# Performance work log

Hardware: AMD Instinct MI355X
Metric: run time of the kernel (lower is better)

## Reference

```python
import jax, jax.numpy as jnp
import numpy as np

B, NPG = 64, 512          # graphs, nodes per graph
N_TOTAL = B * NPG
LIG = 128                 # ligand nodes per graph (segment 0); rest are protein (segment 1)
BOX = 40.0                # Angstrom box for random coords -> realistic radius-graph density
INTER_CUTOFF = 10.0       # normalize_coord is identity (scale=1)
INTRA_CUTOFF = 8.0


def setup_inputs() -> dict:
    key = jax.random.key(0)
    X = jax.random.uniform(key, (N_TOTAL, 1, 3), dtype=jnp.float32) * BOX
    batch_id = jnp.repeat(jnp.arange(B, dtype=jnp.int32), NPG)
    local = jnp.tile(jnp.arange(NPG, dtype=jnp.int32), B)
    segment_id = (local >= LIG).astype(jnp.int32)
    is_global = jnp.logical_or(local == 0, local == LIG)  # one global node per segment
    return {"X": X, "batch_id": batch_id, "segment_id": segment_id, "is_global": is_global}


def _radial_edges(X, src_dst, cutoff):
    # src_dst: [E, 2] node indices; X: [N, C, 3], channel 0 holds coords
    p = X[:, 0][src_dst]                              # [E, 2, 3]
    dist = jnp.linalg.norm(p[:, 0] - p[:, 1], axis=-1)
    return src_dst[dist <= cutoff].T                  # [2, E']


def reference(X, batch_id, segment_id, is_global):
    N = batch_id.shape[0]
    nB = int(batch_id[-1]) + 1
    lengths = jax.ops.segment_sum(jnp.ones_like(batch_id), batch_id, num_segments=nB)
    max_n = int(jnp.max(lengths))
    offsets = jnp.concatenate([jnp.zeros((1,), lengths.dtype), jnp.cumsum(lengths)[:-1]])
    gni = jnp.arange(N)
    gni2lni = gni - offsets[batch_id]                 # local node index within its graph

    # Dense [N, max_n] same-batch mask via cumsum trick (O(N*max_n))
    same_bid = jnp.zeros((N, max_n), jnp.float32)
    same_bid = same_bid.at[gni, lengths[batch_id] - 1].set(1.0)
    same_bid = 1.0 - jnp.cumsum(same_bid, axis=-1)
    same_bid = jnp.concatenate([jnp.ones((N, 1), jnp.float32), same_bid[:, :-1]], axis=-1)
    same_bid = same_bid.at[gni, gni2lni].set(0.0)     # remove self edges

    row, col = jnp.nonzero(same_bid)                  # all same-graph candidate pairs
    col = col + offsets[batch_id[row]]                # local col -> global node index

    row_global = is_global[row]
    col_global = is_global[col]
    not_global = jnp.logical_not(jnp.logical_or(row_global, col_global))
    row_seg = segment_id[row]
    col_seg = segment_id[col]

    # intra-protein context edges (segment 1, within 8A)
    sel = (row_seg == col_seg) & (row_seg == 1) & not_global
    ctx_edges = _radial_edges(X, jnp.stack([row[sel], col[sel]], axis=1), INTRA_CUTOFF)

    # inter ligand-protein edges (within 10A)
    sel = (row_seg != col_seg) & not_global
    ir, ic = row[sel], col[sel]
    inter_edges = _radial_edges(X, jnp.stack([ir, ic], axis=1), INTER_CUTOFF)
    if inter_edges.shape[1] == 0:
        inter_edges = jnp.array([[ir[0], ic[0]], [ic[0], ir[0]]], dtype=inter_edges.dtype)

    reduced_inter_edge_batchid = batch_id[inter_edges[0][inter_edges[0] < inter_edges[1]]]
    reduced_inter_edge_offsets = offsets[reduced_inter_edge_batchid]

    # global<->same-segment edges and global<->global edges appended to context
    sel = (row_seg == col_seg) & jnp.logical_not(not_global)
    global_normal = jnp.stack([row[sel], col[sel]])
    sel = row_global & col_global
    global_global = jnp.stack([row[sel], col[sel]])
    ctx_edges = jnp.concatenate([ctx_edges, global_normal, global_global], axis=1)

    return ctx_edges, inter_edges, reduced_inter_edge_batchid, reduced_inter_edge_offsets
```

## Files before the change

kernel.cpp:

```cpp
#include <hip/hip_runtime.h>

#define NB 64
#define NPG 512
#define LIG 128
#define NBLK 2048
#define RPB 16
#define THREADS 256
typedef unsigned long long ull;

__device__ __forceinline__ float dist2(float dx, float dy, float dz) {
    return __fadd_rn(__fadd_rn(__fmul_rn(dx, dx), __fmul_rn(dy, dy)), __fmul_rn(dz, dz));
}
#define T10 __uint_as_float(0x42C80001u)
#define T8  __uint_as_float(0x42800001u)

__global__ __launch_bounds__(THREADS) void count_kernel(const float* __restrict__ X,
                                                        ull* __restrict__ gmask,
                                                        int* __restrict__ bp) {
    __shared__ float s[NPG * 3];
    __shared__ ull smask[RPB * 8];
    __shared__ int rcs[RPB], ris[RPB];
    const int b = blockIdx.x;
    const int g = b >> 5;
    const int sg = b & 31;
    const int t = threadIdx.x;
    const int lane = t & 63;
    const int w = t >> 6;
    for (int i = t; i < 384; i += THREADS)
        ((float4*)s)[i] = ((const float4*)X)[g * 384 + i];
    if (t < RPB * 8) smask[t] = 0ull;
    __syncthreads();

    float cx[8], cy[8], cz[8];
#pragma unroll
    for (int k = 0; k < 8; ++k) {
        const int c = k * 64 + lane;
        cx[k] = s[3 * c]; cy[k] = s[3 * c + 1]; cz[k] = s[3 * c + 2];
    }

#pragma unroll
    for (int j = 0; j < 4; ++j) {
        const int lr = w * 4 + j;
        const int r = sg * 16 + lr;
        const float px = s[3 * r], py = s[3 * r + 1], pz = s[3 * r + 2];
        int cc = 0, ci = 0;
        if (sg < 8) {
            if (r != 0) {
                ull mm[6];
#pragma unroll
                for (int k = 2; k < 8; ++k) {
                    ull m = __ballot(dist2(px - cx[k], py - cy[k], pz - cz[k]) <= T10);
                    if (k == 2) m &= ~1ull;
                    mm[k - 2] = m;
                    ci += __popcll(m);
                }
                if (lane == 0) {
#pragma unroll
                    for (int k = 0; k < 6; ++k) smask[lr * 8 + 2 + k] = mm[k];
                }
            }
        } else if (r != LIG) {
            ull mm[8];
#pragma unroll
            for (int k = 0; k < 2; ++k) {
                ull m = __ballot(dist2(px - cx[k], py - cy[k], pz - cz[k]) <= T10);
                if (k == 0) m &= ~1ull;
                mm[k] = m;
                ci += __popcll(m);
            }
            const int kr = r >> 6;
            const ull selfbit = 1ull << (r & 63);
#pragma unroll
            for (int k = 2; k < 8; ++k) {
                ull m = __ballot(dist2(px - cx[k], py - cy[k], pz - cz[k]) <= T8);
                if (k == 2) m &= ~1ull;
                if (k == kr) m &= ~selfbit;
                mm[k] = m;
                cc += __popcll(m);
            }
            if (lane == 0) {
#pragma unroll
                for (int k = 0; k < 8; ++k) smask[lr * 8 + k] = mm[k];
            }
        }
        if (lane == 0) { rcs[lr] = cc; ris[lr] = ci; }
    }
    __syncthreads();
    if (t < RPB * 8) gmask[(size_t)b * (RPB * 8) + t] = smask[t];
    if (t < RPB) {
        int c = rcs[t], i = ris[t];
#pragma unroll
        for (int off = 8; off >= 1; off >>= 1) {
            c += __shfl_down(c, off, 64);
            i += __shfl_down(i, off, 64);
        }
        if (t == 0) {
            bp[b] = c;
            bp[NBLK + b] = i;
            bp[2 * NBLK + b] = (sg < 8) ? i : 0;
        }
    }
}

__global__ __launch_bounds__(THREADS) void emit_kernel(const ull* __restrict__ gmask,
                                                       const int* __restrict__ bp,
                                                       int* __restrict__ out) {
    __shared__ ull smask[RPB * 8];
    __shared__ int sc[RPB], si[RPB];
    __shared__ int blkb[3], tot[3], sint;
    const int b = blockIdx.x;
    const int g = b >> 5;
    const int sg = b & 31;
    const int t = threadIdx.x;
    const int lane = t & 63;
    const int w = t >> 6;
    const ull lmask = (1ull << lane) - 1ull;
    const int gn = g * NPG;

    if (t < RPB * 8) smask[t] = gmask[(size_t)b * (RPB * 8) + t];

    if (w < 3) {
        const int4* bp4 = (const int4*)(bp + w * NBLK);
        int v[32]; int sum = 0;
#pragma unroll
        for (int i = 0; i < 8; ++i) {
            const int4 q = bp4[lane * 8 + i];
            v[4 * i + 0] = q.x; v[4 * i + 1] = q.y; v[4 * i + 2] = q.z; v[4 * i + 3] = q.w;
            sum += q.x + q.y + q.z + q.w;
        }
        int incl = sum;
#pragma unroll
        for (int off = 1; off < 64; off <<= 1) {
            const int n = __shfl_up(incl, off, 64);
            if (lane >= off) incl += n;
        }
        if (lane == (b >> 5)) {
            int e = incl - sum;
            const int idx = b & 31;
            for (int i = 0; i < idx; ++i) e += v[i];
            blkb[w] = e;
        }
        if (lane == 63) tot[w] = incl;
    }
    __syncthreads();

    if (t < RPB) {
        int mc = 0, mi = 0;
        if (sg < 8) {
#pragma unroll
            for (int k = 2; k < 8; ++k) mi += __popcll(smask[t * 8 + k]);
        } else {
            mi = __popcll(smask[t * 8 + 0]) + __popcll(smask[t * 8 + 1]);
#pragma unroll
            for (int k = 2; k < 8; ++k) mc += __popcll(smask[t * 8 + k]);
        }
        int ic = mc, ii = mi;
#pragma unroll
        for (int off = 1; off < RPB; off <<= 1) {
            const int a0 = __shfl_up(ic, off, 64);
            const int a1 = __shfl_up(ii, off, 64);
            if (lane >= off) { ic += a0; ii += a1; }
        }
        sc[t] = blkb[0] + ic - mc;
        si[t] = blkb[1] + ii - mi;
        if (t == RPB - 1) sint = ii;
    }
    __syncthreads();

    const int Eci = tot[0];
    const int Ei  = tot[1];
    const int Er  = tot[2];
    const int Ectx = Eci + NB * 1020 + NB * 2;

    int* ctx_src   = out;
    int* ctx_dst   = out + Ectx;
    int* inter_src = out + 2 * Ectx;
    int* inter_dst = inter_src + Ei;
    int* red_bid   = out + 2 * Ectx + 2 * Ei;
    int* red_off   = red_bid + Er;

    for (int j = 0; j < 4; ++j) {
        const int lr = w * 4 + j;
        const int r = sg * 16 + lr;
        const int row = gn + r;

        ull m[8];
#pragma unroll
        for (int k = 0; k < 8; ++k) m[k] = smask[lr * 8 + k];

        if (sg < 8) {
            if (r == 0) {
                for (int k = 0; k < 2; ++k) {
                    const int c = k * 64 + lane;
                    if (c >= 1 && c < LIG) {
                        const int pos = Eci + g * 1020 + (c - 1);
                        ctx_src[pos] = row; ctx_dst[pos] = gn + c;
                    }
                }
                if (lane == 0) {
                    const int pos = Eci + NB * 1020 + g * 2;
                    ctx_src[pos] = row; ctx_dst[pos] = gn + LIG;
                }
            } else {
                int ib = si[lr];
#pragma unroll
                for (int k = 2; k < 8; ++k) {
                    if (m[k]) {
                        if ((m[k] >> lane) & 1ull) {
                            const int c = k * 64 + lane;
                            const int p = __popcll(m[k] & lmask);
                            inter_src[ib + p] = row; inter_dst[ib + p] = gn + c;
                        }
                        ib += __popcll(m[k]);
                    }
                }
                if (lane == 0) {
                    const int pos = Eci + g * 1020 + (LIG - 1) + (r - 1);
                    ctx_src[pos] = row; ctx_dst[pos] = gn;
                }
            }
        } else {
            if (r == LIG) {
                for (int k = 2; k < 8; ++k) {
                    const int c = k * 64 + lane;
                    if (c > LIG) {
                        const int pos = Eci + g * 1020 + 2 * (LIG - 1) + (c - LIG - 1);
                        ctx_src[pos] = row; ctx_dst[pos] = gn + c;
                    }
                }
                if (lane == 0) {
                    const int pos = Eci + NB * 1020 + g * 2 + 1;
                    ctx_src[pos] = row; ctx_dst[pos] = gn;
                }
            } else {
                int ib = si[lr];
#pragma unroll
                for (int k = 0; k < 2; ++k) {
                    if (m[k]) {
                        if ((m[k] >> lane) & 1ull) {
                            const int c = k * 64 + lane;
                            const int pos = ib + __popcll(m[k] & lmask);
                            inter_src[pos] = row; inter_dst[pos] = gn + c;
                        }
                        ib += __popcll(m[k]);
                    }
                }
                int cb = sc[lr];
#pragma unroll
                for (int k = 2; k < 8; ++k) {
                    if (m[k]) {
                        if ((m[k] >> lane) & 1ull) {
                            const int c = k * 64 + lane;
                            const int pos = cb + __popcll(m[k] & lmask);
                            ctx_src[pos] = row; ctx_dst[pos] = gn + c;
                        }
                        cb += __popcll(m[k]);
                    }
                }
                if (lane == 0) {
                    const int pos = Eci + g * 1020 + 2 * (LIG - 1) + (NPG - LIG - 1) + (r - LIG - 1);
                    ctx_src[pos] = row; ctx_dst[pos] = gn + LIG;
                }
            }
        }
    }

    if (sg < 8) {
        const int rb0 = blkb[2];
        const int n = sint;
        for (int i = t; i < n; i += THREADS) {
            red_bid[rb0 + i] = g;
            red_off[rb0 + i] = gn;
        }
    }
}

extern "C" void kernel_launch(void* const* d_in, const int* in_sizes, int n_in,
                              void* d_out, int out_size, void* d_ws, size_t ws_size,
                              hipStream_t stream) {
    (void)in_sizes; (void)n_in; (void)out_size; (void)ws_size;
    const float* X = (const float*)d_in[0];
    int* ws = (int*)d_ws;
    int* bp = ws;
    ull* gmask = (ull*)(ws + 3 * NBLK + 64);
    int* out = (int*)d_out;

    count_kernel<<<NBLK, THREADS, 0, stream>>>(X, gmask, bp);
    emit_kernel<<<NBLK, THREADS, 0, stream>>>(gmask, bp, out);
}
```

Baseline: 83.90 us.

## Move block-offset scan into last count block via atomic ticket; use larger blocks

Each count block now writes its masks straight to global memory and atomically takes a ticket. The last block to finish scans all per-block counts once and stores exclusive offsets and totals, so emit blocks no longer each rescan the whole count array. Blocks grow to 512 threads covering 32 rows, which halves the block count. The change adds a memset launch, an atomic serialization point and a single-block tail scan inside count_kernel.

```diff
diff --git a/kernel.cpp b/kernel.cpp
--- a/kernel.cpp
+++ b/kernel.cpp
@@ -3,9 +3,9 @@
 #define NB 64
 #define NPG 512
 #define LIG 128
-#define NBLK 2048
-#define RPB 16
-#define THREADS 256
+#define NBLK 1024
+#define RPB 32
+#define THREADS 512
 typedef unsigned long long ull;
 
 __device__ __forceinline__ float dist2(float dx, float dy, float dz) {
@@ -16,19 +16,20 @@
 
 __global__ __launch_bounds__(THREADS) void count_kernel(const float* __restrict__ X,
                                                         ull* __restrict__ gmask,
-                                                        int* __restrict__ bp) {
+                                                        int* __restrict__ bp,
+                                                        unsigned int* __restrict__ ticket,
+                                                        int* __restrict__ bb,
+                                                        int* __restrict__ totals) {
     __shared__ float s[NPG * 3];
-    __shared__ ull smask[RPB * 8];
     __shared__ int rcs[RPB], ris[RPB];
+    __shared__ int amLast;
     const int b = blockIdx.x;
-    const int g = b >> 5;
-    const int sg = b & 31;
+    const int g = b >> 4;
+    const int h = b & 15;
     const int t = threadIdx.x;
     const int lane = t & 63;
     const int w = t >> 6;
-    for (int i = t; i < 384; i += THREADS)
-        ((float4*)s)[i] = ((const float4*)X)[g * 384 + i];
-    if (t < RPB * 8) smask[t] = 0ull;
+    if (t < 384) ((float4*)s)[t] = ((const float4*)X)[g * 384 + t];
     __syncthreads();
 
     float cx[8], cy[8], cz[8];
@@ -38,13 +39,14 @@
         cx[k] = s[3 * c]; cy[k] = s[3 * c + 1]; cz[k] = s[3 * c + 2];
     }
 
+    ull* gm = gmask + (size_t)b * (RPB * 8);
 #pragma unroll
     for (int j = 0; j < 4; ++j) {
         const int lr = w * 4 + j;
-        const int r = sg * 16 + lr;
+        const int r = h * 32 + lr;
         const float px = s[3 * r], py = s[3 * r + 1], pz = s[3 * r + 2];
         int cc = 0, ci = 0;
-        if (sg < 8) {
+        if (h < 4) {
             if (r != 0) {
                 ull mm[6];
 #pragma unroll
@@ -56,61 +58,96 @@
                 }
                 if (lane == 0) {
 #pragma unroll
-                    for (int k = 0; k < 6; ++k) smask[lr * 8 + 2 + k] = mm[k];
-                }
+                    for (int k = 0; k < 6; ++k) gm[lr * 8 + 2 + k] = mm[k];
+                }
+            } else if (lane == 0) {
+#pragma unroll
+                for (int k = 2; k < 8; ++k) gm[lr * 8 + k] = 0ull;
             }
-        } else if (r != LIG) {
-            ull mm[8];
-#pragma unroll
-            for (int k = 0; k < 2; ++k) {
-                ull m = __ballot(dist2(px - cx[k], py - cy[k], pz - cz[k]) <= T10);
-                if (k == 0) m &= ~1ull;
-                mm[k] = m;
-                ci += __popcll(m);
+        } else {
+            if (r != LIG) {
+                ull mm[8];
+#pragma unroll
+                for (int k = 0; k < 2; ++k) {
+                    ull m = __ballot(dist2(px - cx[k], py - cy[k], pz - cz[k]) <= T10);
+                    if (k == 0) m &= ~1ull;
+                    mm[k] = m;
+                    ci += __popcll(m);
+                }
+                const int kr = r >> 6;
+                const ull selfbit = 1ull << (r & 63);
+#pragma unroll
+                for (int k = 2; k < 8; ++k) {
+                    ull m = __ballot(dist2(px - cx[k], py - cy[k], pz - cz[k]) <= T8);
+                    if (k == 2) m &= ~1ull;
+                    if (k == kr) m &= ~selfbit;
+                    mm[k] = m;
+                    cc += __popcll(m);
+                }
+                if (lane == 0) {
+#pragma unroll
+                    for (int k = 0; k < 8; ++k) gm[lr * 8 + k] = mm[k];
+                }
+            } else if (lane == 0) {
+#pragma unroll
+                for (int k = 0; k < 8; ++k) gm[lr * 8 + k] = 0ull;
             }
-            const int kr = r >> 6;
-            const ull selfbit = 1ull << (r & 63);
-#pragma unroll
-            for (int k = 2; k < 8; ++k) {
-                ull m = __ballot(dist2(px - cx[k], py - cy[k], pz - cz[k]) <= T8);
-                if (k == 2) m &= ~1ull;
-                if (k == kr) m &= ~selfbit;
-                mm[k] = m;
-                cc += __popcll(m);
-            }
-            if (lane == 0) {
-#pragma unroll
-                for (int k = 0; k < 8; ++k) smask[lr * 8 + k] = mm[k];
-            }
         }
         if (lane == 0) { rcs[lr] = cc; ris[lr] = ci; }
     }
     __syncthreads();
-    if (t < RPB * 8) gmask[(size_t)b * (RPB * 8) + t] = smask[t];
-    if (t < RPB) {
-        int c = rcs[t], i = ris[t];
-#pragma unroll
-        for (int off = 8; off >= 1; off >>= 1) {
+
+    if (t < 64) {
+        int c = (t < RPB) ? rcs[t] : 0;
+        int i = (t < RPB) ? ris[t] : 0;
+#pragma unroll
+        for (int off = 16; off >= 1; off >>= 1) {
             c += __shfl_down(c, off, 64);
             i += __shfl_down(i, off, 64);
         }
         if (t == 0) {
-            bp[b] = c;
-            bp[NBLK + b] = i;
-            bp[2 * NBLK + b] = (sg < 8) ? i : 0;
-        }
+            __hip_atomic_store(&bp[b], c, __ATOMIC_RELAXED, __HIP_MEMORY_SCOPE_AGENT);
+            __hip_atomic_store(&bp[NBLK + b], i, __ATOMIC_RELAXED, __HIP_MEMORY_SCOPE_AGENT);
+            __hip_atomic_store(&bp[2 * NBLK + b], (h < 4) ? i : 0, __ATOMIC_RELAXED, __HIP_MEMORY_SCOPE_AGENT);
+            const unsigned int old =
+                __hip_atomic_fetch_add(ticket, 1u, __ATOMIC_ACQ_REL, __HIP_MEMORY_SCOPE_AGENT);
+            amLast = (old == NBLK - 1u);
+        }
+    }
+    __syncthreads();
+    if (!amLast) return;
+
+    if (w < 3) {
+        const int base = w * NBLK + lane * 16;
+        int v[16]; int sum = 0;
+#pragma unroll
+        for (int i = 0; i < 16; ++i) {
+            v[i] = __hip_atomic_load(&bp[base + i], __ATOMIC_RELAXED, __HIP_MEMORY_SCOPE_AGENT);
+            sum += v[i];
+        }
+        int incl = sum;
+#pragma unroll
+        for (int off = 1; off < 64; off <<= 1) {
+            const int n = __shfl_up(incl, off, 64);
+            if (lane >= off) incl += n;
+        }
+        int e = incl - sum;
+#pragma unroll
+        for (int i = 0; i < 16; ++i) { bb[base + i] = e; e += v[i]; }
+        if (lane == 63) totals[w] = incl;
     }
 }
 
 __global__ __launch_bounds__(THREADS) void emit_kernel(const ull* __restrict__ gmask,
-                                                       const int* __restrict__ bp,
+                                                       const int* __restrict__ bb,
+                                                       const int* __restrict__ totals,
                                                        int* __restrict__ out) {
     __shared__ ull smask[RPB * 8];
     __shared__ int sc[RPB], si[RPB];
     __shared__ int blkb[3], tot[3], sint;
     const int b = blockIdx.x;
-    const int g = b >> 5;
-    const int sg = b & 31;
+    const int g = b >> 4;
+    const int h = b & 15;
     const int t = threadIdx.x;
     const int lane = t & 63;
     const int w = t >> 6;
@@ -118,35 +155,12 @@
     const int gn = g * NPG;
 
     if (t < RPB * 8) smask[t] = gmask[(size_t)b * (RPB * 8) + t];
-
-    if (w < 3) {
-        const int4* bp4 = (const int4*)(bp + w * NBLK);
-        int v[32]; int sum = 0;
-#pragma unroll
-        for (int i = 0; i < 8; ++i) {
-            const int4 q = bp4[lane * 8 + i];
-            v[4 * i + 0] = q.x; v[4 * i + 1] = q.y; v[4 * i + 2] = q.z; v[4 * i + 3] = q.w;
-            sum += q.x + q.y + q.z + q.w;
-        }
-        int incl = sum;
-#pragma unroll
-        for (int off = 1; off < 64; off <<= 1) {
-            const int n = __shfl_up(incl, off, 64);
-            if (lane >= off) incl += n;
-        }
-        if (lane == (b >> 5)) {
-            int e = incl - sum;
-            const int idx = b & 31;
-            for (int i = 0; i < idx; ++i) e += v[i];
-            blkb[w] = e;
-        }
-        if (lane == 63) tot[w] = incl;
-    }
+    if (t < 3) { blkb[t] = bb[t * NBLK + b]; tot[t] = totals[t]; }
     __syncthreads();
 
     if (t < RPB) {
         int mc = 0, mi = 0;
-        if (sg < 8) {
+        if (h < 4) {
 #pragma unroll
             for (int k = 2; k < 8; ++k) mi += __popcll(smask[t * 8 + k]);
         } else {
@@ -181,14 +195,14 @@
 
     for (int j = 0; j < 4; ++j) {
         const int lr = w * 4 + j;
-        const int r = sg * 16 + lr;
+        const int r = h * 32 + lr;
         const int row = gn + r;
 
         ull m[8];
 #pragma unroll
         for (int k = 0; k < 8; ++k) m[k] = smask[lr * 8 + k];
 
-        if (sg < 8) {
+        if (h < 4) {
             if (r == 0) {
                 for (int k = 0; k < 2; ++k) {
                     const int c = k * 64 + lane;
@@ -265,7 +279,7 @@
         }
     }
 
-    if (sg < 8) {
+    if (h < 4) {
         const int rb0 = blkb[2];
         const int n = sint;
         for (int i = t; i < n; i += THREADS) {
@@ -282,9 +296,13 @@
     const float* X = (const float*)d_in[0];
     int* ws = (int*)d_ws;
     int* bp = ws;
-    ull* gmask = (ull*)(ws + 3 * NBLK + 64);
+    unsigned int* ticket = (unsigned int*)(ws + 3 * NBLK);
+    int* totals = ws + 3 * NBLK + 16;
+    int* bb = ws + 4096;
+    ull* gmask = (ull*)(ws + 8192);
     int* out = (int*)d_out;
 
-    count_kernel<<<NBLK, THREADS, 0, stream>>>(X, gmask, bp);
-    emit_kernel<<<NBLK, THREADS, 0, stream>>>(gmask, bp, out);
+    hipMemsetAsync(ticket, 0, sizeof(unsigned int), stream);
+    count_kernel<<<NBLK, THREADS, 0, stream>>>(X, gmask, bp, ticket, bb, totals);
+    emit_kernel<<<NBLK, THREADS, 0, stream>>>(gmask, bb, totals, out);
 }
```

Result: slower. 111.6 us (+33.0%).
